# Kernel tuning notes

Hardware: AMD Instinct MI355X
Metric: run time of the kernel (lower is better)

Reference implementation:

```python
import jax, jax.numpy as jnp
import numpy as np
from jax import lax

TH = 1.0  # fire threshold (init kwarg th)


def setup_inputs() -> dict:
    key = jax.random.key(0)
    k0, k1, k2 = jax.random.split(key, 3)
    B, T, C = 32, 3000, 512
    hs_pad = jax.random.normal(k0, (B, T, C), dtype=jnp.float32)
    hs_mask = jnp.ones((B, 1, T), dtype=jnp.int32)  # espnet-style [B,1,T] mask, 1=valid
    # Conv1d(C, C, k=5) weight layout [out, in, k], fan-in scaled
    conv_w = jax.random.normal(k1, (C, C, 5), dtype=jnp.float32) * (1.0 / np.sqrt(C * 5))
    conv_b = jnp.zeros((C,), dtype=jnp.float32)
    # Linear(C, 1): stored transposed as [C, 1]
    lin_w = jax.random.normal(k2, (C, 1), dtype=jnp.float32) * (1.0 / np.sqrt(C))
    lin_b = jnp.zeros((1,), dtype=jnp.float32)
    return dict(hs_pad=hs_pad, hs_mask=hs_mask, conv_w=conv_w, conv_b=conv_b,
                lin_w=lin_w, lin_b=lin_b)


def _cif_single(alpha, h, th):
    """Integrate-and-fire for one sequence. alpha:[T], h:[T,C] -> [T,C] (zero padded)."""
    T, C = h.shape

    def step(carry, inp):
        acc, hacc = carry
        a, hu = inp
        acc2 = acc + a
        fired = acc2 >= th
        a1 = th - acc  # = th - (acc2 - a)
        emit = jnp.where(fired, hacc + a1 * hu, jnp.zeros_like(hu))
        new_acc = jnp.where(fired, a - a1, acc2)
        new_h = jnp.where(fired, (a - a1) * hu, hacc + a * hu)
        return (new_acc, new_h), (fired, emit)

    (acc_f, h_f), (fired, emits) = lax.scan(
        step, (jnp.float32(0.0), jnp.zeros((C,), h.dtype)), (alpha, h))
    nfire = jnp.cumsum(fired.astype(jnp.int32))
    idx = jnp.where(fired, nfire - 1, T)  # non-fired steps dump into scratch row T
    out = jnp.zeros((T + 1, C), h.dtype).at[idx].add(emits)
    # tail emission: remaining mass >= th/2
    tail = acc_f >= th * 0.5
    tail_idx = jnp.where(tail, nfire[-1], T)
    out = out.at[tail_idx].add(jnp.where(tail, h_f, jnp.zeros_like(h_f)))
    return out[:T]  # fires <= T always (alpha < 1 = th)


def _forward(hs_pad, hs_mask, conv_w, conv_b, lin_w, lin_b):
    B, T, C = hs_pad.shape
    # Conv1d(C,C,5,pad=2) on [B,C,T]  (note: self.norm is never used in the torch forward)
    x = lax.conv_general_dilated(hs_pad.transpose(0, 2, 1), conv_w, (1,), [(2, 2)],
                                 dimension_numbers=('NCH', 'OIH', 'NCH'))
    x = jax.nn.relu(x + conv_b[None, :, None])  # [B,C,T]
    alpha = jax.nn.sigmoid(jnp.einsum('bct,co->bto', x, lin_w) + lin_b)  # [B,T,1]
    # ys_pad=None -> T_y = 0; loss computed BEFORE masking (as in torch)
    loss_pen = jnp.abs(alpha.sum(axis=1) - 0.0).sum()
    a = alpha[..., 0] * (hs_mask[:, 0, :] != 0).astype(alpha.dtype)  # masked_fill(mask==0, 0)
    cs = jax.vmap(lambda av, hv: _cif_single(av, hv, TH))(a, hs_pad)  # [B,T,C]
    cs_mask = jnp.any(cs != 0.0, axis=-1)[:, None, :]  # [B,1,T]
    return cs, cs_mask, loss_pen


def reference(hs_pad, hs_mask, conv_w, conv_b, lin_w, lin_b):
    return _forward(hs_pad, hs_mask, conv_w, conv_b, lin_w, lin_b)
```

## Files before the change

kernel.cpp:

```cpp
#include <hip/hip_runtime.h>
#include <math.h>

#define B_ 32
#define T_ 3000
#define C_ 512
#define THf 1.0f
#define KW 2560

typedef _Float16 f16;
typedef _Float16 half8 __attribute__((ext_vector_type(8)));
typedef float floatx4 __attribute__((ext_vector_type(4)));

#define GLOBAL_AS __attribute__((address_space(1)))
#define LDS_AS __attribute__((address_space(3)))

#define CS_SIZE  ((size_t)B_ * T_ * C_)
#define MASK_OFF CS_SIZE
#define LOSS_OFF (CS_SIZE + (size_t)B_ * T_)

#define LOSC 64.0f

#define WHI_OFF   0
#define WLO_OFF   2621440
#define PL_OFF    5242880
#define ALPHA_OFF 8314880
#define SEGI_OFF  8698880
#define SEGW_OFF  9466880
#define TOT_OFF   10234880

__global__ __launch_bounds__(256) void w_prep_kernel(
    const float* __restrict__ W, f16* __restrict__ whi, f16* __restrict__ wlo)
{
    int idx = blockIdx.x * 256 + threadIdx.x;
    if (idx >= 512 * KW) return;
    int ie = idx & 7;
    int o  = (idx >> 3) & 511;
    int i8 = (idx >> 12) & 63;
    int k  = idx >> 18;
    int i  = i8 * 8 + ie;
    float w = W[o * KW + i * 5 + k];
    f16 h = (f16)w;
    whi[idx] = h;
    wlo[idx] = (f16)((w - (float)h) * LOSC);
}

__global__ __launch_bounds__(256, 3) void conv_alpha_mfma_a(
    const float* __restrict__ hs, const f16* __restrict__ whi_g,
    const f16* __restrict__ wlo_g, const float* __restrict__ conv_b,
    const float* __restrict__ lin_w, float* __restrict__ pl)
{
    __shared__ f16 sm[2][8704];

    int tid  = threadIdx.x;
    int orig = blockIdx.x;
    int bid  = (orig & 7) * 384 + (orig >> 3);
    int nb  = bid & 3;
    int mtg = bid >> 2;
    int b   = mtg / 24;
    int mt  = mtg - b * 24;
    int t0  = mt * 128;

    int wid = tid >> 6, l = tid & 63;
    int wm = wid >> 1, wn = wid & 1;
    int l15 = l & 15, l4 = l >> 4;
    int o0 = nb * 128;

    const float* hb = hs + (size_t)b * T_ * C_;

    floatx4 acc[4][4];
#pragma unroll
    for (int mf = 0; mf < 4; ++mf)
#pragma unroll
        for (int nf = 0; nf < 4; ++nf) acc[mf][nf] = (floatx4)0.f;

    float4 sA[3][2];
    auto stage_load = [&](int icn) {
#pragma unroll
        for (int u = 0; u < 3; ++u) {
            int j = tid + u * 256;
            float4 z = make_float4(0.f, 0.f, 0.f, 0.f);
            sA[u][0] = z; sA[u][1] = z;
            if (j < 544) {
                int r = j >> 2, c = j & 3;
                int t = t0 - 2 + r;
                if ((unsigned)t < 3000u) {
                    const float4* p =
                        (const float4*)(hb + (size_t)t * C_ + icn * 32 + c * 8);
                    sA[u][0] = p[0];
                    sA[u][1] = p[1];
                }
            }
        }
    };
    auto stage_write = [&](int abuf) {
#pragma unroll
        for (int u = 0; u < 3; ++u) {
            int j = tid + u * 256;
            if (j < 544) {
                int r = j >> 2, c = j & 3;
                float vv[8] = {sA[u][0].x, sA[u][0].y, sA[u][0].z, sA[u][0].w,
                               sA[u][1].x, sA[u][1].y, sA[u][1].z, sA[u][1].w};
                half8 hh, ll;
#pragma unroll
                for (int q = 0; q < 8; ++q) {
                    f16 x = (f16)vv[q];
                    hh[q] = x;
                    ll[q] = (f16)((vv[q] - (float)x) * LOSC);
                }
                f16* base = &sm[abuf][0] + r * 64;
                int swz = r & 7;
                *(half8*)(base + (((c)     ^ swz) << 3)) = hh;
                *(half8*)(base + (((c + 4) ^ swz) << 3)) = ll;
            }
        }
    };

    const f16* whiL = whi_g + ((l4 * 512) + o0 + wn * 64 + l15) * 8;
    const f16* wloL = wlo_g + ((l4 * 512) + o0 + wn * 64 + l15) * 8;

    const f16 inv64 = (f16)0.015625f;

    half8 bh[4], bl[4];

    stage_load(0);
#pragma unroll
    for (int nf = 0; nf < 4; ++nf) {
        bh[nf] = *(const half8*)(whiL + nf * 128);
        bl[nf] = *(const half8*)(wloL + nf * 128);
    }
    stage_write(0);
    __syncthreads();

#define CONV_STEP(KK)                                                         \
    do {                                                                      \
        const int kk_ = (KK);                                                 \
        const int kcur_ = kk_ % 5;                                            \
        const int bufc_ = (kk_ < 5) ? 0 : 1;                                  \
        if (kk_ == 0) stage_load(icB);                                        \
        if (kk_ == 3) stage_write(1);                                         \
        if (kk_ == 5) stage_load((icA + 2 <= 15) ? icA + 2 : 15);             \
        if (kk_ == 8) stage_write(0);                                         \
        {                                                                     \
            const f16* Ab_ = &sm[bufc_][0];                                   \
            int m7_ = (l15 + kcur_) & 7;                                      \
            int sh_ = (l4 ^ m7_) * 8;                                         \
            int sl_ = ((l4 + 4) ^ m7_) * 8;                                   \
            __builtin_amdgcn_s_setprio(1);                                    \
            _Pragma("unroll")                                                 \
            for (int mf = 0; mf < 4; ++mf) {                                  \
                int r_ = wm * 64 + mf * 16 + l15 + kcur_;                     \
                half8 ah = *(const half8*)(Ab_ + r_ * 64 + sh_);              \
                half8 al = *(const half8*)(Ab_ + r_ * 64 + sl_);              \
                half8 ahd = ah * inv64;                                       \
                half8 ald = al * inv64;                                       \
                _Pragma("unroll")                                             \
                for (int nf = 0; nf < 4; ++nf) {                              \
                    acc[mf][nf] = __builtin_amdgcn_mfma_f32_16x16x32_f16(     \
                        ah, bh[nf], acc[mf][nf], 0, 0, 0);                    \
                    acc[mf][nf] = __builtin_amdgcn_mfma_f32_16x16x32_f16(     \
                        ald, bh[nf], acc[mf][nf], 0, 0, 0);                   \
                    acc[mf][nf] = __builtin_amdgcn_mfma_f32_16x16x32_f16(     \
                        ahd, bl[nf], acc[mf][nf], 0, 0, 0);                   \
                }                                                             \
            }                                                                 \
            __builtin_amdgcn_s_setprio(0);                                    \
        }                                                                     \
        {     \
            int nic_ = (kk_ + 1 < 5) ? icA                                    \
                       : ((kk_ + 1 < 10) ? icB                                \
                                         : ((icA + 2 <= 15) ? icA + 2 : 15)); \
            int nk_ = (kk_ + 1) % 5;                                          \
            int st_ = (nk_ * 64 + nic_ * 4) * 4096;                           \
            _Pragma("unroll")                                                 \
            for (int nf = 0; nf < 4; ++nf) {                                  \
                bh[nf] = *(const half8*)(whiL + st_ + nf * 128);              \
                bl[nf] = *(const half8*)(wloL + st_ + nf * 128);              \
            }                                                                 \
        }                                                                     \
        if (kk_ == 4 || kk_ == 9) __syncthreads();                            \
    } while (0)

    for (int ic2 = 0; ic2 < 8; ++ic2) {
        int icA = ic2 * 2;
        int icB = icA + 1;
        CONV_STEP(0);
        CONV_STEP(1);
        CONV_STEP(2);
        CONV_STEP(3);
        CONV_STEP(4);
        CONV_STEP(5);
        CONV_STEP(6);
        CONV_STEP(7);
        CONV_STEP(8);
        CONV_STEP(9);
    }
#undef CONV_STEP

    float cb[4], lw[4];
#pragma unroll
    for (int nf = 0; nf < 4; ++nf) {
        int o = o0 + wn * 64 + nf * 16 + l15;
        cb[nf] = conv_b[o];
        lw[nf] = lin_w[o];
    }
    float* plb = pl + (size_t)(nb * 2 + wn) * (B_ * T_) + b * T_;
#pragma unroll
    for (int mf = 0; mf < 4; ++mf) {
#pragma unroll
        for (int reg = 0; reg < 4; ++reg) {
            float v = 0.f;
#pragma unroll
            for (int nf = 0; nf < 4; ++nf) {
                float c = acc[mf][nf][reg];
                v += fmaxf(c + cb[nf], 0.f) * lw[nf];
            }
            v += __shfl_xor(v, 1);
            v += __shfl_xor(v, 2);
            v += __shfl_xor(v, 4);
            v += __shfl_xor(v, 8);
            int trow = t0 + wm * 64 + mf * 16 + l4 * 4 + reg;
            if (l15 == reg && trow < T_) plb[trow] = v;
        }
    }
}

__global__ __launch_bounds__(256) void alpha_combine_kernel(
    const float* __restrict__ pl, const float* __restrict__ lin_b,
    float* __restrict__ alpha)
{
    int idx = blockIdx.x * 256 + threadIdx.x;
    if (idx >= B_ * T_) return;
    float s = lin_b[0];
#pragma unroll
    for (int p = 0; p < 8; ++p) s += pl[(size_t)p * (B_ * T_) + idx];
    alpha[idx] = 1.f / (1.f + expf(-s));
}

__global__ __launch_bounds__(64) void scan_kernel(
    float* __restrict__ alpha, const int* __restrict__ mask,
    int2* __restrict__ seg_i, float2* __restrict__ seg_w,
    int* __restrict__ total_rows, float* __restrict__ out_loss)
{
    int lane = threadIdx.x;
    float lsum = 0.f;
    if (lane < B_) {
        const float4* ap = (const float4*)(alpha + lane * T_);
        const int4*   mp = (const int4*)(mask + lane * T_);
        float* astore = alpha + lane * T_;
        int2*   si = seg_i + lane * T_;
        float2* sw = seg_w + lane * T_;

        float acc = 0.f, leftover = 0.f;
        int nf = 0, prev_t = -1;

        float4 c0 = ap[0], c1 = ap[1];
        int4   m0 = mp[0], m1 = mp[1];
        for (int tc = 0; tc < T_ / 8; ++tc) {
            float4 n0, n1; int4 nm0, nm1;
            if (tc + 1 < T_ / 8) {
                n0 = ap[(tc + 1) * 2]; n1 = ap[(tc + 1) * 2 + 1];
                nm0 = mp[(tc + 1) * 2]; nm1 = mp[(tc + 1) * 2 + 1];
            }
            float av[8] = {c0.x, c0.y, c0.z, c0.w, c1.x, c1.y, c1.z, c1.w};
            int   mv[8] = {m0.x, m0.y, m0.z, m0.w, m1.x, m1.y, m1.z, m1.w};
#pragma unroll
            for (int u = 0; u < 8; ++u) {
                int t = tc * 8 + u;
                float araw = av[u];
                lsum += araw;
                float a = (mv[u] != 0) ? araw : 0.f;
                astore[t] = a;
                float acc2 = acc + a;
                float a1 = THf - acc;
                if (acc2 >= THf) {
                    si[nf] = make_int2(prev_t, t);
                    sw[nf] = make_float2(leftover, a1);
                    float rem = a - a1;
                    leftover = rem;
                    acc = rem;
                    prev_t = t;
                    ++nf;
                } else {
                    acc = acc2;
                }
            }
            c0 = n0; c1 = n1; m0 = nm0; m1 = nm1;
        }
        int tot = nf;
        if (acc >= 0.5f * THf) {
            si[nf] = make_int2(prev_t, T_);
            sw[nf] = make_float2(leftover, 0.f);
            ++tot;
        }
        total_rows[lane] = tot;
        lsum = fabsf(lsum);
    }
#pragma unroll
    for (int off = 16; off >= 1; off >>= 1) lsum += __shfl_down(lsum, off);
    if (lane == 0) out_loss[0] = lsum;
}

__global__ __launch_bounds__(128) void emit_kernel(
    const float* __restrict__ hs, const float* __restrict__ alpha,
    const int2* __restrict__ seg_i, const float2* __restrict__ seg_w,
    const int* __restrict__ total_rows, float* __restrict__ out)
{
    int blk = blockIdx.x;
    int b = blk / T_;
    int r = blk % T_;
    int tid = threadIdx.x;

    float4* cs4 = (float4*)(out + ((size_t)b * T_ + r) * C_);
    float* maskp = out + MASK_OFF + (size_t)b * T_ + r;
    int tot = total_rows[b];

    if (r >= tot) {
        float4 z; z.x = 0.f; z.y = 0.f; z.z = 0.f; z.w = 0.f;
        cs4[tid] = z;
        if (tid == 0) *maskp = 0.f;
        return;
    }
    int2   si = seg_i[b * T_ + r];
    float2 sw = seg_w[b * T_ + r];
    const float4* hb = (const float4*)(hs + (size_t)b * T_ * C_);
    const float*  ab = alpha + b * T_;

    float4 acc; acc.x = 0.f; acc.y = 0.f; acc.z = 0.f; acc.w = 0.f;
    int ts = si.x, te = si.y;
    if (ts >= 0) {
        float4 h = hb[(size_t)ts * (C_ / 4) + tid];
        acc.x = sw.x * h.x; acc.y = sw.x * h.y; acc.z = sw.x * h.z; acc.w = sw.x * h.w;
    }
    for (int t = ts + 1; t < te; ++t) {
        float a = ab[t];
        float4 h = hb[(size_t)t * (C_ / 4) + tid];
        acc.x = fmaf(a, h.x, acc.x); acc.y = fmaf(a, h.y, acc.y);
        acc.z = fmaf(a, h.z, acc.z); acc.w = fmaf(a, h.w, acc.w);
    }
    if (te < T_) {
        float4 h = hb[(size_t)te * (C_ / 4) + tid];
        acc.x = fmaf(sw.y, h.x, acc.x); acc.y = fmaf(sw.y, h.y, acc.y);
        acc.z = fmaf(sw.y, h.z, acc.z); acc.w = fmaf(sw.y, h.w, acc.w);
    }
    cs4[tid] = acc;
    if (tid == 0) *maskp = 1.f;
}

extern "C" void kernel_launch(void* const* d_in, const int* in_sizes, int n_in,
                              void* d_out, int out_size, void* d_ws, size_t ws_size,
                              hipStream_t stream)
{
    const float* hs     = (const float*)d_in[0];
    const int*   hmask  = (const int*)d_in[1];
    const float* conv_w = (const float*)d_in[2];
    const float* conv_b = (const float*)d_in[3];
    const float* lin_w  = (const float*)d_in[4];
    const float* lin_b  = (const float*)d_in[5];
    float* out = (float*)d_out;
    char*  ws  = (char*)d_ws;

    f16*    whi   = (f16*)(ws + WHI_OFF);
    f16*    wlo   = (f16*)(ws + WLO_OFF);
    float*  pl    = (float*)(ws + PL_OFF);
    float*  alpha = (float*)(ws + ALPHA_OFF);
    int2*   seg_i = (int2*)(ws + SEGI_OFF);
    float2* seg_w = (float2*)(ws + SEGW_OFF);
    int*    tot   = (int*)(ws + TOT_OFF);

    w_prep_kernel<<<(512 * KW + 255) / 256, 256, 0, stream>>>(conv_w, whi, wlo);
    conv_alpha_mfma_a<<<B_ * 24 * 4, 256, 0, stream>>>(hs, whi, wlo, conv_b,
                                                       lin_w, pl);
    alpha_combine_kernel<<<(B_ * T_ + 255) / 256, 256, 0, stream>>>(pl, lin_b, alpha);
    scan_kernel<<<1, 64, 0, stream>>>(alpha, hmask, seg_i, seg_w, tot, out + LOSS_OFF);
    emit_kernel<<<B_ * T_, 128, 0, stream>>>(hs, alpha, seg_i, seg_w, tot, out);
}
```

Baseline: 993.8 us.

## Stage conv weight fragments through LDS via async global-to-LDS loads

Conv weight hi/lo fragments are no longer loaded by each wave straight from global memory into registers. The block now copies them cooperatively into a double-buffered LDS region with global_load_lds, one K-step ahead, and each wave reads its B fragments from LDS. The input tile drops from double to single buffering, and the unrolled 10-step macro becomes a plain 80-step loop with a barrier after every step. The aim is to stop waves with the same output half from fetching the same weights twice and to overlap weight fetches with MFMA work. In exchange, barriers rise from 16 to 80, LDS use per block grows, and the barriers may force waits on outstanding input prefetch loads.

```diff
diff --git a/kernel.cpp b/kernel.cpp
--- a/kernel.cpp
+++ b/kernel.cpp
@@ -49,7 +49,7 @@
     const f16* __restrict__ wlo_g, const float* __restrict__ conv_b,
     const float* __restrict__ lin_w, float* __restrict__ pl)
 {
-    __shared__ f16 sm[2][8704];
+    __shared__ f16 sm[25088];
 
     int tid  = threadIdx.x;
     int orig = blockIdx.x;
@@ -92,7 +92,7 @@
             }
         }
     };
-    auto stage_write = [&](int abuf) {
+    auto stage_write = [&]() {
 #pragma unroll
         for (int u = 0; u < 3; ++u) {
             int j = tid + u * 256;
@@ -107,7 +107,7 @@
                     hh[q] = x;
                     ll[q] = (f16)((vv[q] - (float)x) * LOSC);
                 }
-                f16* base = &sm[abuf][0] + r * 64;
+                f16* base = sm + r * 64;
                 int swz = r & 7;
                 *(half8*)(base + (((c)     ^ swz) << 3)) = hh;
                 *(half8*)(base + (((c + 4) ^ swz) << 3)) = ll;
@@ -115,86 +115,73 @@
         }
     };
 
-    const f16* whiL = whi_g + ((l4 * 512) + o0 + wn * 64 + l15) * 8;
-    const f16* wloL = wlo_g + ((l4 * 512) + o0 + wn * 64 + l15) * 8;
+    auto issue_w = [&](int s2) {
+        int buf = s2 & 1;
+        int ic2 = s2 / 5, k2 = s2 - ic2 * 5;
+#pragma unroll
+        for (int rr = 0; rr < 4; ++rr) {
+            int r = wid * 4 + rr;
+            int arr = r >> 3, kc = (r >> 1) & 3, oh = r & 1;
+            const f16* gsrc = (arr ? wlo_g : whi_g) +
+                ((size_t)((k2 * 64 + ic2 * 4 + kc) * 512 + o0 + oh * 64 + l)) * 8;
+            f16* ldst = sm + 8704 + (buf * 2 + arr) * 4096 + (kc * 128 + oh * 64) * 8;
+            __builtin_amdgcn_global_load_lds((const GLOBAL_AS void*)gsrc,
+                                             (LDS_AS void*)ldst, 16, 0, 0);
+        }
+    };
 
     const f16 inv64 = (f16)0.015625f;
 
-    half8 bh[4], bl[4];
-
     stage_load(0);
-#pragma unroll
-    for (int nf = 0; nf < 4; ++nf) {
-        bh[nf] = *(const half8*)(whiL + nf * 128);
-        bl[nf] = *(const half8*)(wloL + nf * 128);
-    }
-    stage_write(0);
+    stage_write();
+    issue_w(0);
     __syncthreads();
 
-#define CONV_STEP(KK)                                                         \
-    do {                                                                      \
-        const int kk_ = (KK);                                                 \
-        const int kcur_ = kk_ % 5;                                            \
-        const int bufc_ = (kk_ < 5) ? 0 : 1;                                  \
-        if (kk_ == 0) stage_load(icB);                                        \
-        if (kk_ == 3) stage_write(1);                                         \
-        if (kk_ == 5) stage_load((icA + 2 <= 15) ? icA + 2 : 15);             \
-        if (kk_ == 8) stage_write(0);                                         \
-        {                                                                     \
-            const f16* Ab_ = &sm[bufc_][0];                                   \
-            int m7_ = (l15 + kcur_) & 7;                                      \
-            int sh_ = (l4 ^ m7_) * 8;                                         \
-            int sl_ = ((l4 + 4) ^ m7_) * 8;                                   \
-            __builtin_amdgcn_s_setprio(1);                                    \
-            _Pragma("unroll")                                                 \
-            for (int mf = 0; mf < 4; ++mf) {                                  \
-                int r_ = wm * 64 + mf * 16 + l15 + kcur_;                     \
-                half8 ah = *(const half8*)(Ab_ + r_ * 64 + sh_);              \
-                half8 al = *(const half8*)(Ab_ + r_ * 64 + sl_);              \
-                half8 ahd = ah * inv64;                                       \
-                half8 ald = al * inv64;                                       \
-                _Pragma("unroll")                                             \
-                for (int nf = 0; nf < 4; ++nf) {                              \
-                    acc[mf][nf] = __builtin_amdgcn_mfma_f32_16x16x32_f16(     \
-                        ah, bh[nf], acc[mf][nf], 0, 0, 0);                    \
-                    acc[mf][nf] = __builtin_amdgcn_mfma_f32_16x16x32_f16(     \
-                        ald, bh[nf], acc[mf][nf], 0, 0, 0);                   \
-                    acc[mf][nf] = __builtin_amdgcn_mfma_f32_16x16x32_f16(     \
-                        ahd, bl[nf], acc[mf][nf], 0, 0, 0);                   \
-                }                                                             \
-            }                                                                 \
-            __builtin_amdgcn_s_setprio(0);                                    \
-        }                                                                     \
-        {     \
-            int nic_ = (kk_ + 1 < 5) ? icA                                    \
-                       : ((kk_ + 1 < 10) ? icB                                \
-                                         : ((icA + 2 <= 15) ? icA + 2 : 15)); \
-            int nk_ = (kk_ + 1) % 5;                                          \
-            int st_ = (nk_ * 64 + nic_ * 4) * 4096;                           \
-            _Pragma("unroll")                                                 \
-            for (int nf = 0; nf < 4; ++nf) {                                  \
-                bh[nf] = *(const half8*)(whiL + st_ + nf * 128);              \
-                bl[nf] = *(const half8*)(wloL + st_ + nf * 128);              \
-            }                                                                 \
-        }                                                                     \
-        if (kk_ == 4 || kk_ == 9) __syncthreads();                            \
-    } while (0)
-
-    for (int ic2 = 0; ic2 < 8; ++ic2) {
-        int icA = ic2 * 2;
-        int icB = icA + 1;
-        CONV_STEP(0);
-        CONV_STEP(1);
-        CONV_STEP(2);
-        CONV_STEP(3);
-        CONV_STEP(4);
-        CONV_STEP(5);
-        CONV_STEP(6);
-        CONV_STEP(7);
-        CONV_STEP(8);
-        CONV_STEP(9);
-    }
-#undef CONV_STEP
+    for (int s = 0; s < 80; ++s) {
+        int ic = s / 5, k = s - ic * 5;
+        int wbuf = s & 1;
+
+        if (k == 0 && ic > 0) {
+            stage_write();
+            __syncthreads();
+        }
+        if (s + 1 < 80) issue_w(s + 1);
+        if (k == 2 && ic + 1 < 16) stage_load(ic + 1);
+
+        const f16* Wh = sm + 8704 + (wbuf * 2 + 0) * 4096;
+        const f16* Wl = sm + 8704 + (wbuf * 2 + 1) * 4096;
+        int m7 = (l15 + k) & 7;
+        int sh = (l4 ^ m7) * 8;
+        int sl = ((l4 + 4) ^ m7) * 8;
+
+        half8 bh[4], bl[4];
+#pragma unroll
+        for (int f = 0; f < 4; ++f) {
+            int wrow = l4 * 128 + wn * 64 + f * 16 + l15;
+            bh[f] = *(const half8*)(Wh + wrow * 8);
+            bl[f] = *(const half8*)(Wl + wrow * 8);
+        }
+        __builtin_amdgcn_s_setprio(1);
+#pragma unroll
+        for (int mf = 0; mf < 4; ++mf) {
+            int r = wm * 64 + mf * 16 + l15 + k;
+            half8 ah = *(const half8*)(sm + r * 64 + sh);
+            half8 al = *(const half8*)(sm + r * 64 + sl);
+            half8 ahd = ah * inv64;
+            half8 ald = al * inv64;
+#pragma unroll
+            for (int nf = 0; nf < 4; ++nf) {
+                acc[mf][nf] = __builtin_amdgcn_mfma_f32_16x16x32_f16(
+                    ah, bh[nf], acc[mf][nf], 0, 0, 0);
+                acc[mf][nf] = __builtin_amdgcn_mfma_f32_16x16x32_f16(
+                    ald, bh[nf], acc[mf][nf], 0, 0, 0);
+                acc[mf][nf] = __builtin_amdgcn_mfma_f32_16x16x32_f16(
+                    ahd, bl[nf], acc[mf][nf], 0, 0, 0);
+            }
+        }
+        __builtin_amdgcn_s_setprio(0);
+        __syncthreads();
+    }
 
     float cb[4], lw[4];
 #pragma unroll
```

Result: faster. 958.1 us (-3.6%).
